# Kernel tuning notes

Hardware: AMD Instinct MI355X
Metric: run time of the kernel (lower is better)

The kernel has to match this reference:

```python
import jax, jax.numpy as jnp
import numpy as np
import math

B, S, HID, H = 4, 4096, 1024, 16
DH = HID // H  # 64

def setup_inputs() -> dict:
    key = jax.random.key(0)
    ks = jax.random.split(key, 6)
    query = jax.random.normal(ks[0], (B, S, HID), dtype=jnp.float32)
    key_t = jax.random.normal(ks[1], (B, S, HID), dtype=jnp.float32)
    value = jax.random.normal(ks[2], (B, S, HID), dtype=jnp.float32)
    attn_mask = jax.random.normal(ks[3], (B, S, H, H), dtype=jnp.float32)
    # nn.Linear(hidden, 3*hidden): weight (3H, H), bias (3H,)
    W_qkv = jax.random.normal(ks[4], (3 * HID, HID), dtype=jnp.float32) * (1.0 / math.sqrt(HID))
    b_qkv = jax.random.normal(ks[5], (3 * HID,), dtype=jnp.float32) * 0.01
    return {"query": query, "key": key_t, "value": value, "attn_mask": attn_mask,
            "W_qkv": W_qkv, "b_qkv": b_qkv}

def reference(query, key, value, attn_mask, W_qkv, b_qkv):
    # fused QKV projection (only `query` is used, matching the source)
    qkv = jnp.einsum('bsh,oh->bso', query, W_qkv) + b_qkv  # (B,S,3*HID)
    q, k, v = jnp.split(qkv, 3, axis=-1)
    q = q.reshape(B, S, H, DH)
    k = k.reshape(B, S, H, DH)
    v = v.reshape(B, S, H, DH)
    # NOTE: no (B,H,S,D) permute in the source -> scores are head-vs-head per position
    scale = 1.0 / math.sqrt(DH)
    qk = jnp.einsum('bshd,bsgd->bshg', q, k) * scale + attn_mask  # (B,S,H,H)
    attn_weight = jax.nn.softmax(qk, axis=-1)
    # dropout_p=0 (eval): identity
    o = jnp.einsum('bshg,bsgd->bshd', attn_weight, v)  # (B,S,H,DH)
    return o.reshape(B, S, HID)
```

## Files before the change

### kernel.cpp

```cpp
#include <hip/hip_runtime.h>
#include <cstdint>
#include <cstddef>


typedef __attribute__((ext_vector_type(8))) short bf16x8;
typedef __attribute__((ext_vector_type(4))) float f32x4;

__device__ inline unsigned short f2bf(float f) {
  unsigned int i = __float_as_uint(f);
  i += 0x7fff + ((i >> 16) & 1);
  return (unsigned short)(i >> 16);
}

__device__ inline void async16(const void* g, void* l) {
  __builtin_amdgcn_global_load_lds(
      (const __attribute__((address_space(1))) void*)g,
      (__attribute__((address_space(3))) void*)l, 16, 0, 0);
}

__device__ inline void unpack8(bf16x8 v, float* f) {
  union { bf16x8 s; unsigned int u[4]; } x; x.s = v;
  #pragma unroll
  for (int i = 0; i < 4; ++i) {
    f[2 * i]     = __uint_as_float(x.u[i] << 16);
    f[2 * i + 1] = __uint_as_float(x.u[i] & 0xffff0000u);
  }
}

__global__ __launch_bounds__(256) void cast_kernel(const float* __restrict__ in,
                                                   unsigned short* __restrict__ out,
                                                   int n) {
  int i = (blockIdx.x * 256 + threadIdx.x) * 4;
  if (i >= n) return;
  float4 v = *(const float4*)(in + i);
  union { unsigned short u[4]; unsigned long long ll; } o;
  o.u[0] = f2bf(v.x); o.u[1] = f2bf(v.y); o.u[2] = f2bf(v.z); o.u[3] = f2bf(v.w);
  *(unsigned long long*)(out + i) = o.ll;
}

#define GK 1024
#define GN 3072
__global__ __launch_bounds__(512, 2) void gemm_qkv(const unsigned short* __restrict__ A,
                                                   const unsigned short* __restrict__ Bm,
                                                   const float* __restrict__ bias,
                                                   unsigned short* __restrict__ C) {
  __shared__ unsigned short As[2][256][64];
  __shared__ unsigned short Bs[2][256][64];

  const int bid = blockIdx.x;
  const int swz = (bid & 7) * 96 + (bid >> 3);
  const int m0 = (swz / 12) * 256;
  const int n0 = (swz % 12) * 256;

  const int tid  = threadIdx.x;
  const int lane = tid & 63;
  const int wave = tid >> 6;
  const int wm = wave & 1;
  const int wn = wave >> 1;
  const int fr = lane & 15;
  const int fq = lane >> 4;

  const int r0 = tid >> 3;
  const int c0 = (tid & 7) ^ (r0 & 7);
  const unsigned short* gA = A  + (size_t)(m0 + r0) * GK + c0 * 8;
  const unsigned short* gB = Bm + (size_t)(n0 + r0) * GK + c0 * 8;
  const int ls0 = wave * 512;

#define STAGE_A(tt, hh) do {                                                   \
    unsigned short* lb_ = &As[(tt) & 1][(hh) * 128][0];                        \
    const unsigned short* g_ = gA + (size_t)(hh) * 128 * GK + (tt) * 64;       \
    async16(g_, lb_ + ls0);                                                    \
    async16(g_ + (size_t)64 * GK, lb_ + 4096 + ls0);                           \
  } while (0)
#define STAGE_B(tt, hh) do {                                                   \
    unsigned short* lb_ = &Bs[(tt) & 1][(hh) * 128][0];                        \
    const unsigned short* g_ = gB + (size_t)(hh) * 128 * GK + (tt) * 64;       \
    async16(g_, lb_ + ls0);                                                    \
    async16(g_ + (size_t)64 * GK, lb_ + 4096 + ls0);                           \
  } while (0)

  f32x4 acc[8][4] = {};

  STAGE_A(0, 0); STAGE_A(0, 1); STAGE_B(0, 0); STAGE_B(0, 1);
  STAGE_B(1, 0); STAGE_A(1, 0); STAGE_B(1, 1);

  for (int t = 0; t < 16; ++t) {
    const int cur = t & 1;
    if (t == 0)       { asm volatile("s_waitcnt vmcnt(6)" ::: "memory"); }
    else if (t == 15) { asm volatile("s_waitcnt vmcnt(0)" ::: "memory"); }
    else              { asm volatile("s_waitcnt vmcnt(8)" ::: "memory"); }
    __builtin_amdgcn_s_barrier();
    __builtin_amdgcn_sched_barrier(0);

    bf16x8 bfr[4][2];
    #pragma unroll
    for (int p = 0; p < 4; ++p) {
      bf16x8 af[2][2];
      #pragma unroll
      for (int ii = 0; ii < 2; ++ii) {
        const int rA = (p * 2 + ii) * 32 + wm * 16 + fr;
        #pragma unroll
        for (int ks = 0; ks < 2; ++ks)
          af[ii][ks] = *(const bf16x8*)&As[cur][rA][((ks * 4 + fq) ^ (rA & 7)) * 8];
      }
      if (p == 0) {
        #pragma unroll
        for (int j = 0; j < 4; ++j) {
          const int rB = wn * 64 + j * 16 + fr;
          #pragma unroll
          for (int ks = 0; ks < 2; ++ks)
            bfr[j][ks] = *(const bf16x8*)&Bs[cur][rB][((ks * 4 + fq) ^ (rB & 7)) * 8];
        }
        if (t + 1 < 16) { STAGE_A(t + 1, 1); }
      }
      if (p == 1) {
        asm volatile("s_waitcnt vmcnt(8)" ::: "memory");
      }
      if (p == 2 && t + 2 < 16) { STAGE_B(t + 2, 0); }
      if (p == 3 && t + 2 < 16) { STAGE_A(t + 2, 0); STAGE_B(t + 2, 1); }

      __builtin_amdgcn_s_barrier();
      __builtin_amdgcn_sched_barrier(0);
      __builtin_amdgcn_s_setprio(1);
      #pragma unroll
      for (int ks = 0; ks < 2; ++ks)
        #pragma unroll
        for (int ii = 0; ii < 2; ++ii)
          #pragma unroll
          for (int j = 0; j < 4; ++j)
            acc[p * 2 + ii][j] = __builtin_amdgcn_mfma_f32_16x16x32_bf16(
                af[ii][ks], bfr[j][ks], acc[p * 2 + ii][j], 0, 0, 0);
      __builtin_amdgcn_s_setprio(0);
      __builtin_amdgcn_sched_barrier(0);
    }
  }
#undef STAGE_A
#undef STAGE_B

  #pragma unroll
  for (int i = 0; i < 8; ++i) {
    #pragma unroll
    for (int j = 0; j < 4; ++j) {
      const int col = n0 + wn * 64 + j * 16 + fr;
      const float bc = bias[col];
      const int rowb = m0 + i * 32 + wm * 16 + fq * 4;
      #pragma unroll
      for (int rr = 0; rr < 4; ++rr)
        C[(size_t)(rowb + rr) * GN + col] = f2bf(acc[i][j][rr] + bc);
    }
  }
}

__global__ __launch_bounds__(256) void attn_kernel(const unsigned short* __restrict__ QKV,
                                                   const float* __restrict__ mask,
                                                   float* __restrict__ out) {
  __shared__ unsigned short shKV[4][2048];
  const int wave = threadIdx.x >> 6;
  const int lane = threadIdx.x & 63;
  const int pos = blockIdx.x * 4 + wave;

  const unsigned short* row = QKV + (size_t)pos * 3072;

  #pragma unroll
  for (int t = 0; t < 4; ++t)
    async16(&row[1024 + t * 512 + (size_t)lane * 8], &shKV[wave][t * 512]);

  bf16x8 q0 = *(const bf16x8*)&row[lane * 16];
  bf16x8 q1 = *(const bf16x8*)&row[lane * 16 + 8];

  const int h = lane >> 2;
  const int dg = lane & 3;

  const float* mrow = mask + (size_t)pos * 256 + h * 16;
  float4 m4[4];
  #pragma unroll
  for (int t = 0; t < 4; ++t) m4[t] = *(const float4*)&mrow[t * 4];

  float q[16];
  unpack8(q0, q);
  unpack8(q1, q + 8);

  asm volatile("s_waitcnt vmcnt(0)" ::: "memory");

  float s[16];
  #pragma unroll
  for (int g = 0; g < 16; ++g) {
    const unsigned short* kp = &shKV[wave][g * 64 + dg * 16];
    float kf[16];
    unpack8(*(const bf16x8*)kp, kf);
    unpack8(*(const bf16x8*)(kp + 8), kf + 8);
    float acc = 0.f;
    #pragma unroll
    for (int d = 0; d < 16; ++d) acc += q[d] * kf[d];
    s[g] = acc;
  }
  #pragma unroll
  for (int g = 0; g < 16; ++g) {
    s[g] += __shfl_xor(s[g], 1);
    s[g] += __shfl_xor(s[g], 2);
  }

  const float* mp = (const float*)m4;
  float mx = -1e30f;
  #pragma unroll
  for (int g = 0; g < 16; ++g) {
    s[g] = s[g] * 0.125f + mp[g];
    mx = fmaxf(mx, s[g]);
  }
  float sum = 0.f;
  #pragma unroll
  for (int g = 0; g < 16; ++g) { s[g] = __expf(s[g] - mx); sum += s[g]; }
  float inv = 1.f / sum;

  float o[16];
  #pragma unroll
  for (int dd = 0; dd < 16; ++dd) o[dd] = 0.f;
  #pragma unroll
  for (int g = 0; g < 16; ++g) {
    const unsigned short* vp = &shKV[wave][1024 + g * 64 + dg * 16];
    float vf[16];
    unpack8(*(const bf16x8*)vp, vf);
    unpack8(*(const bf16x8*)(vp + 8), vf + 8);
    float p = s[g];
    #pragma unroll
    for (int dd = 0; dd < 16; ++dd) o[dd] += p * vf[dd];
  }

  float* op = out + (size_t)pos * 1024 + lane * 16;
  #pragma unroll
  for (int t = 0; t < 4; ++t) {
    float4 w;
    w.x = o[t * 4 + 0] * inv; w.y = o[t * 4 + 1] * inv;
    w.z = o[t * 4 + 2] * inv; w.w = o[t * 4 + 3] * inv;
    *(float4*)(op + t * 4) = w;
  }
}

extern "C" void kernel_launch(void* const* d_in, const int* in_sizes, int n_in,
                              void* d_out, int out_size, void* d_ws, size_t ws_size,
                              hipStream_t stream) {
  const float* query = (const float*)d_in[0];
  const float* mask  = (const float*)d_in[3];
  const float* Wqkv  = (const float*)d_in[4];
  const float* bqkv  = (const float*)d_in[5];
  float* out = (float*)d_out;

  unsigned short* qb   = (unsigned short*)d_ws;
  unsigned short* wb   = (unsigned short*)((char*)d_ws + 33554432);
  unsigned short* qkvb = (unsigned short*)((char*)d_ws + 39845888);

  cast_kernel<<<16384, 256, 0, stream>>>(query, qb, 16777216);
  cast_kernel<<<3072, 256, 0, stream>>>(Wqkv, wb, 3145728);

  gemm_qkv<<<768, 512, 0, stream>>>(qb, wb, bqkv, qkvb);

  attn_kernel<<<4096, 256, 0, stream>>>(qkvb, mask, out);
}
```

Baseline: 331.6 us.

## Compute per-position head attention with MFMA instead of scalar dot products

```diff
diff --git a/kernel.cpp b/kernel.cpp
--- a/kernel.cpp
+++ b/kernel.cpp
@@ -4,6 +4,7 @@
 
 
 typedef __attribute__((ext_vector_type(8))) short bf16x8;
+typedef __attribute__((ext_vector_type(4))) short bf16x4;
 typedef __attribute__((ext_vector_type(4))) float f32x4;
 
 __device__ inline unsigned short f2bf(float f) {
@@ -16,15 +17,6 @@
   __builtin_amdgcn_global_load_lds(
       (const __attribute__((address_space(1))) void*)g,
       (__attribute__((address_space(3))) void*)l, 16, 0, 0);
-}
-
-__device__ inline void unpack8(bf16x8 v, float* f) {
-  union { bf16x8 s; unsigned int u[4]; } x; x.s = v;
-  #pragma unroll
-  for (int i = 0; i < 4; ++i) {
-    f[2 * i]     = __uint_as_float(x.u[i] << 16);
-    f[2 * i + 1] = __uint_as_float(x.u[i] & 0xffff0000u);
-  }
 }
 
 __global__ __launch_bounds__(256) void cast_kernel(const float* __restrict__ in,
@@ -151,88 +143,85 @@
   }
 }
 
-__global__ __launch_bounds__(256) void attn_kernel(const unsigned short* __restrict__ QKV,
-                                                   const float* __restrict__ mask,
-                                                   float* __restrict__ out) {
-  __shared__ unsigned short shKV[4][2048];
+__global__ __launch_bounds__(256, 8) void attn_kernel(const unsigned short* __restrict__ QKV,
+                                                      const float* __restrict__ mask,
+                                                      float* __restrict__ out) {
+  __shared__ unsigned short shV[4][1024];
   const int wave = threadIdx.x >> 6;
   const int lane = threadIdx.x & 63;
   const int pos = blockIdx.x * 4 + wave;
 
   const unsigned short* row = QKV + (size_t)pos * 3072;
 
+  async16(&row[2048 + (size_t)lane * 8], &shV[wave][0]);
+  async16(&row[2048 + 512 + (size_t)lane * 8], &shV[wave][512]);
+
+  const int hn  = lane & 15;
+  const int grp = lane >> 4;
+
+  const int qk_off = hn * 64 + grp * 8;
+  bf16x8 qf0 = *(const bf16x8*)&row[qk_off];
+  bf16x8 qf1 = *(const bf16x8*)&row[qk_off + 32];
+  bf16x8 kf0 = *(const bf16x8*)&row[1024 + qk_off];
+  bf16x8 kf1 = *(const bf16x8*)&row[1024 + qk_off + 32];
+
+  float4 mk = *(const float4*)&mask[(size_t)pos * 256 + hn * 16 + grp * 4];
+
+  f32x4 s = {};
+  s = __builtin_amdgcn_mfma_f32_16x16x32_bf16(kf0, qf0, s, 0, 0, 0);
+  s = __builtin_amdgcn_mfma_f32_16x16x32_bf16(kf1, qf1, s, 0, 0, 0);
+
+  float sv0 = s[0] * 0.125f + mk.x;
+  float sv1 = s[1] * 0.125f + mk.y;
+  float sv2 = s[2] * 0.125f + mk.z;
+  float sv3 = s[3] * 0.125f + mk.w;
+  float mx = fmaxf(fmaxf(sv0, sv1), fmaxf(sv2, sv3));
+  mx = fmaxf(mx, __shfl_xor(mx, 16));
+  mx = fmaxf(mx, __shfl_xor(mx, 32));
+  float p0 = __expf(sv0 - mx), p1 = __expf(sv1 - mx);
+  float p2 = __expf(sv2 - mx), p3 = __expf(sv3 - mx);
+  float sum = p0 + p1 + p2 + p3;
+  sum += __shfl_xor(sum, 16);
+  sum += __shfl_xor(sum, 32);
+  const float inv = 1.f / sum;
+
+  union { unsigned u[2]; bf16x4 v; } pa;
+  pa.u[0] = (unsigned)f2bf(p0 * inv) | ((unsigned)f2bf(p1 * inv) << 16);
+  pa.u[1] = (unsigned)f2bf(p2 * inv) | ((unsigned)f2bf(p3 * inv) << 16);
+
+  asm volatile("s_waitcnt vmcnt(0)" ::: "memory");
+
+  float* obase = out + (size_t)pos * 1024 + grp * 256 + hn;
+  const unsigned short* vb = &shV[wave][grp * 256];
   #pragma unroll
-  for (int t = 0; t < 4; ++t)
-    async16(&row[1024 + t * 512 + (size_t)lane * 8], &shKV[wave][t * 512]);
-
-  bf16x8 q0 = *(const bf16x8*)&row[lane * 16];
-  bf16x8 q1 = *(const bf16x8*)&row[lane * 16 + 8];
-
-  const int h = lane >> 2;
-  const int dg = lane & 3;
-
-  const float* mrow = mask + (size_t)pos * 256 + h * 16;
-  float4 m4[4];
-  #pragma unroll
-  for (int t = 0; t < 4; ++t) m4[t] = *(const float4*)&mrow[t * 4];
-
-  float q[16];
-  unpack8(q0, q);
-  unpack8(q1, q + 8);
-
-  asm volatile("s_waitcnt vmcnt(0)" ::: "memory");
-
-  float s[16];
-  #pragma unroll
-  for (int g = 0; g < 16; ++g) {
-    const unsigned short* kp = &shKV[wave][g * 64 + dg * 16];
-    float kf[16];
-    unpack8(*(const bf16x8*)kp, kf);
-    unpack8(*(const bf16x8*)(kp + 8), kf + 8);
-    float acc = 0.f;
+  for (int db = 0; db < 4; ++db) {
+    const int e0 = db * 16 + hn;
+#if __has_builtin(__builtin_amdgcn_mfma_f32_16x16x16bf16_1k)
+    unsigned v0 = vb[e0], v1 = vb[e0 + 64], v2 = vb[e0 + 128], v3 = vb[e0 + 192];
+    union { unsigned u[2]; bf16x4 v; } bfv;
+    bfv.u[0] = v0 | (v1 << 16);
+    bfv.u[1] = v2 | (v3 << 16);
+    f32x4 z = {};
+    f32x4 o4 = __builtin_amdgcn_mfma_f32_16x16x16bf16_1k(pa.v, bfv.v, z, 0, 0, 0);
+#else
+    const int src = grp * 32 + hn;
+    unsigned a0 = __shfl((int)pa.u[0], src), a1 = __shfl((int)pa.u[1], src);
+    unsigned a2 = __shfl((int)pa.u[0], src + 16), a3 = __shfl((int)pa.u[1], src + 16);
+    if (grp >= 2) { a0 = a1 = a2 = a3 = 0; }
+    union { unsigned u[4]; bf16x8 v; } paw;
+    paw.u[0] = a0; paw.u[1] = a1; paw.u[2] = a2; paw.u[3] = a3;
+    const unsigned short* vbf = &shV[wave][((grp & 1) * 8) * 64];
+    unsigned w0 = vbf[e0],       w1 = vbf[e0 + 64],  w2 = vbf[e0 + 128], w3 = vbf[e0 + 192];
+    unsigned w4 = vbf[e0 + 256], w5 = vbf[e0 + 320], w6 = vbf[e0 + 384], w7 = vbf[e0 + 448];
+    union { unsigned u[4]; bf16x8 v; } bfv;
+    bfv.u[0] = w0 | (w1 << 16); bfv.u[1] = w2 | (w3 << 16);
+    bfv.u[2] = w4 | (w5 << 16); bfv.u[3] = w6 | (w7 << 16);
+    f32x4 z = {};
+    f32x4 o4 = __builtin_amdgcn_mfma_f32_16x16x32_bf16(paw.v, bfv.v, z, 0, 0, 0);
+#endif
     #pragma unroll
-    for (int d = 0; d < 16; ++d) acc += q[d] * kf[d];
-    s[g] = acc;
-  }
-  #pragma unroll
-  for (int g = 0; g < 16; ++g) {
-    s[g] += __shfl_xor(s[g], 1);
-    s[g] += __shfl_xor(s[g], 2);
-  }
-
-  const float* mp = (const float*)m4;
-  float mx = -1e30f;
-  #pragma unroll
-  for (int g = 0; g < 16; ++g) {
-    s[g] = s[g] * 0.125f + mp[g];
-    mx = fmaxf(mx, s[g]);
-  }
-  float sum = 0.f;
-  #pragma unroll
-  for (int g = 0; g < 16; ++g) { s[g] = __expf(s[g] - mx); sum += s[g]; }
-  float inv = 1.f / sum;
-
-  float o[16];
-  #pragma unroll
-  for (int dd = 0; dd < 16; ++dd) o[dd] = 0.f;
-  #pragma unroll
-  for (int g = 0; g < 16; ++g) {
-    const unsigned short* vp = &shKV[wave][1024 + g * 64 + dg * 16];
-    float vf[16];
-    unpack8(*(const bf16x8*)vp, vf);
-    unpack8(*(const bf16x8*)(vp + 8), vf + 8);
-    float p = s[g];
-    #pragma unroll
-    for (int dd = 0; dd < 16; ++dd) o[dd] += p * vf[dd];
-  }
-
-  float* op = out + (size_t)pos * 1024 + lane * 16;
-  #pragma unroll
-  for (int t = 0; t < 4; ++t) {
-    float4 w;
-    w.x = o[t * 4 + 0] * inv; w.y = o[t * 4 + 1] * inv;
-    w.z = o[t * 4 + 2] * inv; w.w = o[t * 4 + 3] * inv;
-    *(float4*)(op + t * 4) = w;
+    for (int r = 0; r < 4; ++r)
+      obase[r * 64 + db * 16] = o4[r];
   }
 }
 
```

Result: faster. 318.1 us (-4.1%).
